# Optimization experiments

Measured on AMD Instinct MI355X. Metric: run time of the kernel, lower is better.

Reference implementation:

```python
import jax, jax.numpy as jnp
from jax import lax
import numpy as np

PROPAGATE = 3  # propagate_size; avg_pool2d(3,1,pad=1)*9 == 3x3 zero-padded sum pool
EPS = 1e-07


def setup_inputs() -> dict:
    key = jax.random.key(0)
    k1, k2 = jax.random.split(key)
    foreground = jax.random.normal(k1, (4, 64, 64, 64), dtype=jnp.float32)
    masks = jax.random.uniform(k2, (4, 1, 64, 64), dtype=jnp.float32)
    return {"foreground": foreground, "masks": masks}


def _sum_pool3x3(x):
    # x: [b, p, h, w]; 3x3 stride-1 zero-padded sum (== avg_pool2d(3,1,pad=1) * 9)
    return lax.reduce_window(x, 0.0, lax.add,
                             window_dimensions=(1, 1, PROPAGATE, PROPAGATE),
                             window_strides=(1, 1, 1, 1),
                             padding=[(0, 0), (0, 0), (1, 1), (1, 1)])


def reference(foreground, masks):
    # First-call forward of KnowledgeConsistentAttention (att_scores_prev is None;
    # masks/ratio are only stored as state and do not affect this output).
    bz, nc, h, w = foreground.shape
    # dynamic 1x1 kernels: one kernel per spatial location -> [b, h*w, nc]
    kern = foreground.reshape(bz, nc, h * w).transpose(0, 2, 1) + EPS
    kern = kern / jnp.sqrt(jnp.sum(kern ** 2, axis=-1, keepdims=True))
    # conv2d with per-image 1x1 kernels == per-pixel dot products
    scores = jnp.einsum('bpc,bcyx->bpyx', kern, foreground)  # [b, h*w, h, w]
    scores = _sum_pool3x3(scores)
    att = jax.nn.softmax(scores, axis=1)
    # conv_transpose2d with the same 1x1 kernels == weighted sum of kernels
    out = jnp.einsum('bpc,bpyx->bcyx', kern, att)  # [b, nc, h, w]
    return out
```

## Files before the change

kernel.cpp:

```cpp
#include <hip/hip_runtime.h>


typedef __bf16 bf16_t;
typedef __bf16 bf16x2 __attribute__((ext_vector_type(2)));
typedef __bf16 bf16x8 __attribute__((ext_vector_type(8)));
typedef float f32x4 __attribute__((ext_vector_type(4)));

#define HW_ 4096
#define CH 64

static __device__ __forceinline__ void gload_lds16(const void* gsrc, void* lds_dst) {
  __builtin_amdgcn_global_load_lds(
      (const __attribute__((address_space(1))) unsigned int*)gsrc,
      (__attribute__((address_space(3))) unsigned int*)lds_dst, 16, 0, 0);
}

static __device__ __forceinline__ int pack_bf16x2(float a, float b) {
  bf16x2 p; p[0] = (bf16_t)a; p[1] = (bf16_t)b;
  return __builtin_bit_cast(int, p);
}

__global__ __launch_bounds__(1024, 1) void kca_prep(const float* __restrict__ fg,
                                                    char* __restrict__ KpB,
                                                    char* __restrict__ KBB,
                                                    char* __restrict__ GtB) {
  const int b = blockIdx.x >> 6, y = blockIdx.x & 63;
  const int t = threadIdx.x;
  const float* F = fg + (size_t)b * (CH * HW_);

  __shared__ float  Ft[3 * 64 * 64];
  __shared__ bf16_t Ks[64 * 72];
  __shared__ bf16_t Gs[64 * 72];
  __shared__ float  red[16][64];
  __shared__ float  rn[64];

#pragma unroll
  for (int k = 0; k < 3; ++k) {
    const int o = t + k * 1024;
    const int r = o >> 10, c = (o >> 4) & 63, x4 = o & 15;
    const int gy = y - 1 + r;
    f32x4 v = {0.f, 0.f, 0.f, 0.f};
    if (gy >= 0 && gy <= 63) v = *(const f32x4*)(F + c * HW_ + gy * 64 + x4 * 4);
    *(f32x4*)&Ft[o * 4] = v;
  }
  __syncthreads();

  const int x = t & 63, c0 = t >> 6;
  float v4[4], g4[4], ssq = 0.f;
#pragma unroll
  for (int i = 0; i < 4; ++i) {
    const int c = c0 * 4 + i;
    const float v = Ft[4096 + c * 64 + x] + 1e-7f;
    v4[i] = v; ssq = fmaf(v, v, ssq);
    float s = 0.f;
#pragma unroll
    for (int r = 0; r < 3; ++r) {
      const float* row = &Ft[r * 4096 + c * 64];
      float vv = row[x];
      if (x > 0)  vv += row[x - 1];
      if (x < 63) vv += row[x + 1];
      s += vv;
    }
    g4[i] = s * 1.4426950408889634f;
  }
  red[c0][x] = ssq;
  __syncthreads();
  if (t < 512) red[t >> 6][t & 63] += red[(t >> 6) + 8][t & 63];
  __syncthreads();
  if (t < 256) red[t >> 6][t & 63] += red[(t >> 6) + 4][t & 63];
  __syncthreads();
  if (t < 64) rn[t] = 1.0f / sqrtf(red[0][t] + red[1][t] + red[2][t] + red[3][t]);
  __syncthreads();
  {
    const float rv = rn[x];
    bf16x2* ksp = (bf16x2*)((char*)Ks + x * 144 + c0 * 8);
    bf16x2* gsp = (bf16x2*)((char*)Gs + x * 144 + c0 * 8);
    bf16x2 k0; k0[0] = (bf16_t)(v4[0] * rv); k0[1] = (bf16_t)(v4[1] * rv);
    bf16x2 k1; k1[0] = (bf16_t)(v4[2] * rv); k1[1] = (bf16_t)(v4[3] * rv);
    bf16x2 g0; g0[0] = (bf16_t)g4[0]; g0[1] = (bf16_t)g4[1];
    bf16x2 g1; g1[0] = (bf16_t)g4[2]; g1[1] = (bf16_t)g4[3];
    ksp[0] = k0; ksp[1] = k1;
    gsp[0] = g0; gsp[1] = g1;
  }
  __syncthreads();

  char* Kp_b = KpB + (size_t)b * (HW_ * CH * 2) + (size_t)y * 8192;
  char* Gt_b = GtB + (size_t)b * (HW_ * CH * 2) + (size_t)y * 8192;
  char* KB_b = KBB + (size_t)b * (HW_ * CH * 2);
  if (t < 512) {
    const int row = t >> 3, colb = (t & 7) * 16;
    *(bf16x8*)(Kp_b + row * 128 + colb) = *(const bf16x8*)((char*)Ks + row * 144 + colb);
    const int tile = t >> 8;
    const int mt   = (t >> 6) & 3;
    const int ln   = t & 63;
    const int l15_ = ln & 15, lg_ = ln >> 4;
    bf16x8 kv;
#pragma unroll
    for (int j = 0; j < 8; ++j) {
      const int pl = tile * 32 + 16 * (j >> 2) + 4 * lg_ + (j & 3);
      kv[j] = Ks[pl * 72 + 16 * mt + l15_];
    }
    *(bf16x8*)(KB_b + (size_t)(2 * y + tile) * 4096 + mt * 1024 + ln * 16) = kv;
  } else {
    const int s = t - 512;
    const int row = s >> 3, colb = (s & 7) * 16;
    *(bf16x8*)(Gt_b + row * 128 + colb) = *(const bf16x8*)((char*)Gs + row * 144 + colb);
  }
}

__global__ __launch_bounds__(1024, 4) void kca_attn(const char* __restrict__ KpB,
                                                    const char* __restrict__ KBB,
                                                    const char* __restrict__ GtB,
                                                    float* __restrict__ out,
                                                    float* __restrict__ po1,
                                                    float* __restrict__ lw) {
  const int sw_id = ((blockIdx.x & 7) << 6) | (blockIdx.x >> 3);
  const int h = sw_id >> 8;
  const int b = (sw_id >> 6) & 3, y = sw_id & 63;
  const int t = threadIdx.x;
  const int lane = t & 63, w = t >> 6;
  const int g = w & 7;
  const int st = w >> 3;
  const int l15 = lane & 15, lg = lane >> 4;

  const char* Kp_b = KpB + (size_t)b * (HW_ * CH * 2);
  const char* KB_b = KBB + (size_t)b * (HW_ * CH * 2);
  const char* Gt_b = GtB + (size_t)b * (HW_ * CH * 2);
  float* dstO = (h ? po1 : out) + (size_t)b * (CH * HW_);

  __shared__ __align__(16) char SM[69632];
  __shared__ float mll[8][64];

  char* KpG = SM + g * 8192;

  bf16x8 qb00, qb01, qb10, qb11;
  {
    const char* qr0 = Gt_b + (size_t)(y * 64 + st * 32 + l15) * 128;
    const char* qr1 = qr0 + 16 * 128;
    qb00 = *(const bf16x8*)(qr0 + 16 * lg);
    qb01 = *(const bf16x8*)(qr0 + 64 + 16 * lg);
    qb10 = *(const bf16x8*)(qr1 + 16 * lg);
    qb11 = *(const bf16x8*)(qr1 + 64 + 16 * lg);
  }

  const int cA = st * 128 + lane, cB = cA + 64;
  const int rA1 = cA >> 3, rB1 = cB >> 3;
  const size_t kpoffA = (size_t)rA1 * 128 + (((cA & 7) * 16) ^ ((rA1 & 7) << 4));
  const size_t kpoffB = (size_t)rB1 * 128 + (((cB & 7) * 16) ^ ((rB1 & 7) << 4));

#define STAGE_KP(D, P0)                                                          \
  do {                                                                           \
    gload_lds16(Kp_b + (size_t)(P0) * 128 + kpoffA, KpG + (D) * 4096 + cA * 16); \
    gload_lds16(Kp_b + (size_t)(P0) * 128 + kpoffB, KpG + (D) * 4096 + cB * 16); \
  } while (0)

  f32x4 oaccT[2][4];
#pragma unroll
  for (int s = 0; s < 2; ++s)
#pragma unroll
    for (int mt = 0; mt < 4; ++mt) { oaccT[s][mt][0]=0.f; oaccT[s][mt][1]=0.f; oaccT[s][mt][2]=0.f; oaccT[s][mt][3]=0.f; }
  float lpart0 = 0.f, lpart1 = 0.f;

  const int pb0 = h * 2048 + g * 256;
  STAGE_KP(0, pb0);
  int cur = 0;
  for (int it = 0; it < 8; ++it) {
    __syncthreads();
    const char* kbp = KB_b + (size_t)((pb0 >> 5) + it) * 4096 + lane * 16;
    const bf16x8 kb0 = *(const bf16x8*)(kbp);
    const bf16x8 kb1 = *(const bf16x8*)(kbp + 1024);
    const bf16x8 kb2 = *(const bf16x8*)(kbp + 2048);
    const bf16x8 kb3 = *(const bf16x8*)(kbp + 3072);
    if (it + 1 < 8) STAGE_KP(cur ^ 1, pb0 + (it + 1) * 32);

    const char* kp = KpG + cur * 4096;
    f32x4 S[2][2];
#pragma unroll
    for (int f = 0; f < 2; ++f) {
      const int r = f * 16 + l15, swr = (r & 7) << 4;
      bf16x8 a0 = *(const bf16x8*)(kp + r * 128 + ((16 * lg) ^ swr));
      bf16x8 a1 = *(const bf16x8*)(kp + r * 128 + ((64 + 16 * lg) ^ swr));
      f32x4 z0 = {0.f, 0.f, 0.f, 0.f};
      z0 = __builtin_amdgcn_mfma_f32_16x16x32_bf16(a0, qb00, z0, 0, 0, 0);
      z0 = __builtin_amdgcn_mfma_f32_16x16x32_bf16(a1, qb01, z0, 0, 0, 0);
      S[0][f] = z0;
      f32x4 z1 = {0.f, 0.f, 0.f, 0.f};
      z1 = __builtin_amdgcn_mfma_f32_16x16x32_bf16(a0, qb10, z1, 0, 0, 0);
      z1 = __builtin_amdgcn_mfma_f32_16x16x32_bf16(a1, qb11, z1, 0, 0, 0);
      S[1][f] = z1;
    }

    union { int wd[4]; bf16x8 v; } pa0, pa1;
    {
      const float e0 = exp2f(S[0][0][0]), e1 = exp2f(S[0][0][1]);
      const float e2 = exp2f(S[0][0][2]), e3 = exp2f(S[0][0][3]);
      const float e4 = exp2f(S[0][1][0]), e5 = exp2f(S[0][1][1]);
      const float e6 = exp2f(S[0][1][2]), e7 = exp2f(S[0][1][3]);
      lpart0 += ((e0 + e1) + (e2 + e3)) + ((e4 + e5) + (e6 + e7));
      pa0.wd[0] = pack_bf16x2(e0, e1); pa0.wd[1] = pack_bf16x2(e2, e3);
      pa0.wd[2] = pack_bf16x2(e4, e5); pa0.wd[3] = pack_bf16x2(e6, e7);
    }
    {
      const float e0 = exp2f(S[1][0][0]), e1 = exp2f(S[1][0][1]);
      const float e2 = exp2f(S[1][0][2]), e3 = exp2f(S[1][0][3]);
      const float e4 = exp2f(S[1][1][0]), e5 = exp2f(S[1][1][1]);
      const float e6 = exp2f(S[1][1][2]), e7 = exp2f(S[1][1][3]);
      lpart1 += ((e0 + e1) + (e2 + e3)) + ((e4 + e5) + (e6 + e7));
      pa1.wd[0] = pack_bf16x2(e0, e1); pa1.wd[1] = pack_bf16x2(e2, e3);
      pa1.wd[2] = pack_bf16x2(e4, e5); pa1.wd[3] = pack_bf16x2(e6, e7);
    }

    oaccT[0][0] = __builtin_amdgcn_mfma_f32_16x16x32_bf16(pa0.v, kb0, oaccT[0][0], 0, 0, 0);
    oaccT[1][0] = __builtin_amdgcn_mfma_f32_16x16x32_bf16(pa1.v, kb0, oaccT[1][0], 0, 0, 0);
    oaccT[0][1] = __builtin_amdgcn_mfma_f32_16x16x32_bf16(pa0.v, kb1, oaccT[0][1], 0, 0, 0);
    oaccT[1][1] = __builtin_amdgcn_mfma_f32_16x16x32_bf16(pa1.v, kb1, oaccT[1][1], 0, 0, 0);
    oaccT[0][2] = __builtin_amdgcn_mfma_f32_16x16x32_bf16(pa0.v, kb2, oaccT[0][2], 0, 0, 0);
    oaccT[1][2] = __builtin_amdgcn_mfma_f32_16x16x32_bf16(pa1.v, kb2, oaccT[1][2], 0, 0, 0);
    oaccT[0][3] = __builtin_amdgcn_mfma_f32_16x16x32_bf16(pa0.v, kb3, oaccT[0][3], 0, 0, 0);
    oaccT[1][3] = __builtin_amdgcn_mfma_f32_16x16x32_bf16(pa1.v, kb3, oaccT[1][3], 0, 0, 0);
    cur ^= 1;
  }
#undef STAGE_KP

  lpart0 += __shfl_xor(lpart0, 16); lpart0 += __shfl_xor(lpart0, 32);
  lpart1 += __shfl_xor(lpart1, 16); lpart1 += __shfl_xor(lpart1, 32);
  if (lg == 0) {
    mll[g][st * 32 + l15]      = lpart0;
    mll[g][st * 32 + 16 + l15] = lpart1;
  }
  __syncthreads();
  if (t < 64) {
    float L = 0.f;
#pragma unroll
    for (int k = 0; k < 8; ++k) L += mll[k][t];
    lw[(size_t)((h * 4 + b) * 64 + y) * 64 + t] = L;
  }
  float* Rg = (float*)SM + (g >> 1) * 4352;
  if ((g & 1) == 0) {
#pragma unroll
    for (int s = 0; s < 2; ++s)
#pragma unroll
      for (int mt = 0; mt < 4; ++mt)
#pragma unroll
        for (int r = 0; r < 4; ++r)
          Rg[(16 * mt + l15) * 68 + st * 32 + s * 16 + 4 * lg + r] = oaccT[s][mt][r];
  }
  __syncthreads();
  if (g & 1) {
#pragma unroll
    for (int s = 0; s < 2; ++s)
#pragma unroll
      for (int mt = 0; mt < 4; ++mt)
#pragma unroll
        for (int r = 0; r < 4; ++r)
          Rg[(16 * mt + l15) * 68 + st * 32 + s * 16 + 4 * lg + r] += oaccT[s][mt][r];
  }
  __syncthreads();
  {
    const int c = t >> 4, q4 = (t & 15) * 4;
    const float* R0 = (const float*)SM;
    f32x4 v = *(const f32x4*)(R0 + c * 68 + q4);
    v += *(const f32x4*)(R0 + 4352 + c * 68 + q4);
    v += *(const f32x4*)(R0 + 8704 + c * 68 + q4);
    v += *(const f32x4*)(R0 + 13056 + c * 68 + q4);
    *(f32x4*)(dstO + (size_t)c * HW_ + y * 64 + q4) = v;
  }
}

__global__ __launch_bounds__(256, 8) void kca_reduce(float* __restrict__ out,
                                                     const float* __restrict__ po1,
                                                     const float* __restrict__ lw) {
  const size_t idx = ((size_t)blockIdx.x * 256 + threadIdx.x) * 4;
  const int b = (int)(idx >> 18);
  const int y = (int)((idx >> 6) & 63);
  const int q = (int)(idx & 63);
  const size_t lidx = (size_t)(b * 64 + y) * 64 + q;
  const f32x4 a  = *(const f32x4*)(out + idx);
  const f32x4 p  = *(const f32x4*)(po1 + idx);
  const f32x4 l0 = *(const f32x4*)(lw + lidx);
  const f32x4 l1 = *(const f32x4*)(lw + 16384 + lidx);
  f32x4 o;
#pragma unroll
  for (int j = 0; j < 4; ++j) o[j] = (a[j] + p[j]) * (1.0f / (l0[j] + l1[j]));
  *(f32x4*)(out + idx) = o;
}

extern "C" void kernel_launch(void* const* d_in, const int* in_sizes, int n_in,
                              void* d_out, int out_size, void* d_ws, size_t ws_size,
                              hipStream_t stream) {
  const float* fg = (const float*)d_in[0];
  float* out = (float*)d_out;
  char* ws = (char*)d_ws;
  char* Kp  = ws;
  char* KB  = ws + (2u << 20);
  char* Gt  = ws + (4u << 20);
  float* PO1 = (float*)(ws + (6u << 20));
  float* LW  = (float*)(ws + (10u << 20));
  hipLaunchKernelGGL(kca_prep, dim3(256), dim3(1024), 0, stream, fg, Kp, KB, Gt);
  hipLaunchKernelGGL(kca_attn, dim3(512), dim3(1024), 0, stream, Kp, KB, Gt, out, PO1, LW);
  hipLaunchKernelGGL(kca_reduce, dim3(1024), dim3(256), 0, stream, out, PO1, LW);
}
```

Before: 54.36 us.

## Split attention key range four ways with 256-thread blocks and direct global loads

Restructures the attention kernel from 512 blocks of 1024 threads (two key halves, LDS-staged K tiles via async global-to-LDS loads) to 1024 blocks of 256 threads. Each block covers a quarter of the keys, and each wave handles all 64 query pixels of a row, reading K fragments straight from global/L2. Cross-wave partial sums are combined in a smaller LDS buffer. The reduce kernel now sums four partial outputs and four partial denominators. This drops the per-iteration block barriers and LDS staging and raises block count for better CU spread. In exchange it adds more global/L2 traffic, uses a larger partial-output workspace, and makes the final reduction heavier.

```diff
diff --git a/kernel.cpp b/kernel.cpp
--- a/kernel.cpp
+++ b/kernel.cpp
@@ -8,12 +8,6 @@
 
 #define HW_ 4096
 #define CH 64
-
-static __device__ __forceinline__ void gload_lds16(const void* gsrc, void* lds_dst) {
-  __builtin_amdgcn_global_load_lds(
-      (const __attribute__((address_space(1))) unsigned int*)gsrc,
-      (__attribute__((address_space(3))) unsigned int*)lds_dst, 16, 0, 0);
-}
 
 static __device__ __forceinline__ int pack_bf16x2(float a, float b) {
   bf16x2 p; p[0] = (bf16_t)a; p[1] = (bf16_t)b;
@@ -108,180 +102,147 @@
   }
 }
 
-__global__ __launch_bounds__(1024, 4) void kca_attn(const char* __restrict__ KpB,
-                                                    const char* __restrict__ KBB,
-                                                    const char* __restrict__ GtB,
-                                                    float* __restrict__ out,
-                                                    float* __restrict__ po1,
-                                                    float* __restrict__ lw) {
-  const int sw_id = ((blockIdx.x & 7) << 6) | (blockIdx.x >> 3);
-  const int h = sw_id >> 8;
-  const int b = (sw_id >> 6) & 3, y = sw_id & 63;
+__global__ __launch_bounds__(256, 1) void kca_attn(const char* __restrict__ KpB,
+                                                   const char* __restrict__ KBB,
+                                                   const char* __restrict__ GtB,
+                                                   float* __restrict__ out,
+                                                   float* __restrict__ po,
+                                                   float* __restrict__ lw) {
+  const int sw = ((blockIdx.x & 7) << 7) | (blockIdx.x >> 3);
+  const int h = sw >> 8;
+  const int b = (sw >> 6) & 3, y = sw & 63;
   const int t = threadIdx.x;
   const int lane = t & 63, w = t >> 6;
-  const int g = w & 7;
-  const int st = w >> 3;
   const int l15 = lane & 15, lg = lane >> 4;
 
   const char* Kp_b = KpB + (size_t)b * (HW_ * CH * 2);
   const char* KB_b = KBB + (size_t)b * (HW_ * CH * 2);
   const char* Gt_b = GtB + (size_t)b * (HW_ * CH * 2);
-  float* dstO = (h ? po1 : out) + (size_t)b * (CH * HW_);
-
-  __shared__ __align__(16) char SM[69632];
-  __shared__ float mll[8][64];
-
-  char* KpG = SM + g * 8192;
-
-  bf16x8 qb00, qb01, qb10, qb11;
-  {
-    const char* qr0 = Gt_b + (size_t)(y * 64 + st * 32 + l15) * 128;
-    const char* qr1 = qr0 + 16 * 128;
-    qb00 = *(const bf16x8*)(qr0 + 16 * lg);
-    qb01 = *(const bf16x8*)(qr0 + 64 + 16 * lg);
-    qb10 = *(const bf16x8*)(qr1 + 16 * lg);
-    qb11 = *(const bf16x8*)(qr1 + 64 + 16 * lg);
-  }
-
-  const int cA = st * 128 + lane, cB = cA + 64;
-  const int rA1 = cA >> 3, rB1 = cB >> 3;
-  const size_t kpoffA = (size_t)rA1 * 128 + (((cA & 7) * 16) ^ ((rA1 & 7) << 4));
-  const size_t kpoffB = (size_t)rB1 * 128 + (((cB & 7) * 16) ^ ((rB1 & 7) << 4));
-
-#define STAGE_KP(D, P0)                                                          \
-  do {                                                                           \
-    gload_lds16(Kp_b + (size_t)(P0) * 128 + kpoffA, KpG + (D) * 4096 + cA * 16); \
-    gload_lds16(Kp_b + (size_t)(P0) * 128 + kpoffB, KpG + (D) * 4096 + cB * 16); \
-  } while (0)
-
-  f32x4 oaccT[2][4];
-#pragma unroll
-  for (int s = 0; s < 2; ++s)
-#pragma unroll
-    for (int mt = 0; mt < 4; ++mt) { oaccT[s][mt][0]=0.f; oaccT[s][mt][1]=0.f; oaccT[s][mt][2]=0.f; oaccT[s][mt][3]=0.f; }
-  float lpart0 = 0.f, lpart1 = 0.f;
-
-  const int pb0 = h * 2048 + g * 256;
-  STAGE_KP(0, pb0);
-  int cur = 0;
+
+  __shared__ float Rcomb[2][64 * 72];
+  __shared__ float mll[4][64];
+
+  bf16x8 qb[4][2];
+#pragma unroll
+  for (int qs = 0; qs < 4; ++qs) {
+    const char* qr = Gt_b + (size_t)(y * 64 + qs * 16 + l15) * 128 + 16 * lg;
+    qb[qs][0] = *(const bf16x8*)qr;
+    qb[qs][1] = *(const bf16x8*)(qr + 64);
+  }
+
+  f32x4 oaccT[4][4];
+#pragma unroll
+  for (int qs = 0; qs < 4; ++qs)
+#pragma unroll
+    for (int mt = 0; mt < 4; ++mt) { oaccT[qs][mt][0]=0.f; oaccT[qs][mt][1]=0.f; oaccT[qs][mt][2]=0.f; oaccT[qs][mt][3]=0.f; }
+  float lpart[4] = {0.f, 0.f, 0.f, 0.f};
+
+  const int pbase = h * 1024 + w * 256;
   for (int it = 0; it < 8; ++it) {
-    __syncthreads();
-    const char* kbp = KB_b + (size_t)((pb0 >> 5) + it) * 4096 + lane * 16;
+    const int p0 = pbase + it * 32;
+    const char* kbp = KB_b + (size_t)(p0 >> 5) * 4096 + lane * 16;
     const bf16x8 kb0 = *(const bf16x8*)(kbp);
     const bf16x8 kb1 = *(const bf16x8*)(kbp + 1024);
     const bf16x8 kb2 = *(const bf16x8*)(kbp + 2048);
     const bf16x8 kb3 = *(const bf16x8*)(kbp + 3072);
-    if (it + 1 < 8) STAGE_KP(cur ^ 1, pb0 + (it + 1) * 32);
-
-    const char* kp = KpG + cur * 4096;
-    f32x4 S[2][2];
+
+    union PU { int wd[4]; bf16x8 v; } pa[4];
+
 #pragma unroll
     for (int f = 0; f < 2; ++f) {
-      const int r = f * 16 + l15, swr = (r & 7) << 4;
-      bf16x8 a0 = *(const bf16x8*)(kp + r * 128 + ((16 * lg) ^ swr));
-      bf16x8 a1 = *(const bf16x8*)(kp + r * 128 + ((64 + 16 * lg) ^ swr));
-      f32x4 z0 = {0.f, 0.f, 0.f, 0.f};
-      z0 = __builtin_amdgcn_mfma_f32_16x16x32_bf16(a0, qb00, z0, 0, 0, 0);
-      z0 = __builtin_amdgcn_mfma_f32_16x16x32_bf16(a1, qb01, z0, 0, 0, 0);
-      S[0][f] = z0;
-      f32x4 z1 = {0.f, 0.f, 0.f, 0.f};
-      z1 = __builtin_amdgcn_mfma_f32_16x16x32_bf16(a0, qb10, z1, 0, 0, 0);
-      z1 = __builtin_amdgcn_mfma_f32_16x16x32_bf16(a1, qb11, z1, 0, 0, 0);
-      S[1][f] = z1;
-    }
-
-    union { int wd[4]; bf16x8 v; } pa0, pa1;
-    {
-      const float e0 = exp2f(S[0][0][0]), e1 = exp2f(S[0][0][1]);
-      const float e2 = exp2f(S[0][0][2]), e3 = exp2f(S[0][0][3]);
-      const float e4 = exp2f(S[0][1][0]), e5 = exp2f(S[0][1][1]);
-      const float e6 = exp2f(S[0][1][2]), e7 = exp2f(S[0][1][3]);
-      lpart0 += ((e0 + e1) + (e2 + e3)) + ((e4 + e5) + (e6 + e7));
-      pa0.wd[0] = pack_bf16x2(e0, e1); pa0.wd[1] = pack_bf16x2(e2, e3);
-      pa0.wd[2] = pack_bf16x2(e4, e5); pa0.wd[3] = pack_bf16x2(e6, e7);
-    }
-    {
-      const float e0 = exp2f(S[1][0][0]), e1 = exp2f(S[1][0][1]);
-      const float e2 = exp2f(S[1][0][2]), e3 = exp2f(S[1][0][3]);
-      const float e4 = exp2f(S[1][1][0]), e5 = exp2f(S[1][1][1]);
-      const float e6 = exp2f(S[1][1][2]), e7 = exp2f(S[1][1][3]);
-      lpart1 += ((e0 + e1) + (e2 + e3)) + ((e4 + e5) + (e6 + e7));
-      pa1.wd[0] = pack_bf16x2(e0, e1); pa1.wd[1] = pack_bf16x2(e2, e3);
-      pa1.wd[2] = pack_bf16x2(e4, e5); pa1.wd[3] = pack_bf16x2(e6, e7);
-    }
-
-    oaccT[0][0] = __builtin_amdgcn_mfma_f32_16x16x32_bf16(pa0.v, kb0, oaccT[0][0], 0, 0, 0);
-    oaccT[1][0] = __builtin_amdgcn_mfma_f32_16x16x32_bf16(pa1.v, kb0, oaccT[1][0], 0, 0, 0);
-    oaccT[0][1] = __builtin_amdgcn_mfma_f32_16x16x32_bf16(pa0.v, kb1, oaccT[0][1], 0, 0, 0);
-    oaccT[1][1] = __builtin_amdgcn_mfma_f32_16x16x32_bf16(pa1.v, kb1, oaccT[1][1], 0, 0, 0);
-    oaccT[0][2] = __builtin_amdgcn_mfma_f32_16x16x32_bf16(pa0.v, kb2, oaccT[0][2], 0, 0, 0);
-    oaccT[1][2] = __builtin_amdgcn_mfma_f32_16x16x32_bf16(pa1.v, kb2, oaccT[1][2], 0, 0, 0);
-    oaccT[0][3] = __builtin_amdgcn_mfma_f32_16x16x32_bf16(pa0.v, kb3, oaccT[0][3], 0, 0, 0);
-    oaccT[1][3] = __builtin_amdgcn_mfma_f32_16x16x32_bf16(pa1.v, kb3, oaccT[1][3], 0, 0, 0);
-    cur ^= 1;
-  }
-#undef STAGE_KP
-
-  lpart0 += __shfl_xor(lpart0, 16); lpart0 += __shfl_xor(lpart0, 32);
-  lpart1 += __shfl_xor(lpart1, 16); lpart1 += __shfl_xor(lpart1, 32);
+      const char* ar = Kp_b + (size_t)(p0 + f * 16 + l15) * 128 + 16 * lg;
+      const bf16x8 a0 = *(const bf16x8*)(ar);
+      const bf16x8 a1 = *(const bf16x8*)(ar + 64);
+#pragma unroll
+      for (int qs = 0; qs < 4; ++qs) {
+        f32x4 z = {0.f, 0.f, 0.f, 0.f};
+        z = __builtin_amdgcn_mfma_f32_16x16x32_bf16(a0, qb[qs][0], z, 0, 0, 0);
+        z = __builtin_amdgcn_mfma_f32_16x16x32_bf16(a1, qb[qs][1], z, 0, 0, 0);
+        const float e0 = exp2f(z[0]), e1 = exp2f(z[1]);
+        const float e2 = exp2f(z[2]), e3 = exp2f(z[3]);
+        lpart[qs] += (e0 + e1) + (e2 + e3);
+        pa[qs].wd[2 * f + 0] = pack_bf16x2(e0, e1);
+        pa[qs].wd[2 * f + 1] = pack_bf16x2(e2, e3);
+      }
+    }
+
+#pragma unroll
+    for (int qs = 0; qs < 4; ++qs) {
+      oaccT[qs][0] = __builtin_amdgcn_mfma_f32_16x16x32_bf16(pa[qs].v, kb0, oaccT[qs][0], 0, 0, 0);
+      oaccT[qs][1] = __builtin_amdgcn_mfma_f32_16x16x32_bf16(pa[qs].v, kb1, oaccT[qs][1], 0, 0, 0);
+      oaccT[qs][2] = __builtin_amdgcn_mfma_f32_16x16x32_bf16(pa[qs].v, kb2, oaccT[qs][2], 0, 0, 0);
+      oaccT[qs][3] = __builtin_amdgcn_mfma_f32_16x16x32_bf16(pa[qs].v, kb3, oaccT[qs][3], 0, 0, 0);
+    }
+  }
+
+#pragma unroll
+  for (int qs = 0; qs < 4; ++qs) {
+    lpart[qs] += __shfl_xor(lpart[qs], 16);
+    lpart[qs] += __shfl_xor(lpart[qs], 32);
+  }
   if (lg == 0) {
-    mll[g][st * 32 + l15]      = lpart0;
-    mll[g][st * 32 + 16 + l15] = lpart1;
+#pragma unroll
+    for (int qs = 0; qs < 4; ++qs) mll[w][qs * 16 + l15] = lpart[qs];
+  }
+  float* Rg = &Rcomb[w & 1][0];
+  if (w < 2) {
+#pragma unroll
+    for (int qs = 0; qs < 4; ++qs)
+#pragma unroll
+      for (int mt = 0; mt < 4; ++mt)
+#pragma unroll
+        for (int r = 0; r < 4; ++r)
+          Rg[(16 * mt + l15) * 72 + qs * 16 + 4 * lg + r] = oaccT[qs][mt][r];
+  }
+  __syncthreads();
+  if (w >= 2) {
+#pragma unroll
+    for (int qs = 0; qs < 4; ++qs)
+#pragma unroll
+      for (int mt = 0; mt < 4; ++mt)
+#pragma unroll
+        for (int r = 0; r < 4; ++r)
+          Rg[(16 * mt + l15) * 72 + qs * 16 + 4 * lg + r] += oaccT[qs][mt][r];
   }
   __syncthreads();
   if (t < 64) {
-    float L = 0.f;
-#pragma unroll
-    for (int k = 0; k < 8; ++k) L += mll[k][t];
-    lw[(size_t)((h * 4 + b) * 64 + y) * 64 + t] = L;
-  }
-  float* Rg = (float*)SM + (g >> 1) * 4352;
-  if ((g & 1) == 0) {
-#pragma unroll
-    for (int s = 0; s < 2; ++s)
-#pragma unroll
-      for (int mt = 0; mt < 4; ++mt)
-#pragma unroll
-        for (int r = 0; r < 4; ++r)
-          Rg[(16 * mt + l15) * 68 + st * 32 + s * 16 + 4 * lg + r] = oaccT[s][mt][r];
-  }
-  __syncthreads();
-  if (g & 1) {
-#pragma unroll
-    for (int s = 0; s < 2; ++s)
-#pragma unroll
-      for (int mt = 0; mt < 4; ++mt)
-#pragma unroll
-        for (int r = 0; r < 4; ++r)
-          Rg[(16 * mt + l15) * 68 + st * 32 + s * 16 + 4 * lg + r] += oaccT[s][mt][r];
-  }
-  __syncthreads();
+    const float L = mll[0][t] + mll[1][t] + mll[2][t] + mll[3][t];
+    lw[(size_t)h * 16384 + (size_t)(b * 64 + y) * 64 + t] = L;
+  }
   {
-    const int c = t >> 4, q4 = (t & 15) * 4;
-    const float* R0 = (const float*)SM;
-    f32x4 v = *(const f32x4*)(R0 + c * 68 + q4);
-    v += *(const f32x4*)(R0 + 4352 + c * 68 + q4);
-    v += *(const f32x4*)(R0 + 8704 + c * 68 + q4);
-    v += *(const f32x4*)(R0 + 13056 + c * 68 + q4);
-    *(f32x4*)(dstO + (size_t)c * HW_ + y * 64 + q4) = v;
+    const int c = t >> 2, q16 = (t & 3) * 16;
+    float* dst = (h ? po + (size_t)(h - 1) * 4 * CH * HW_ : out)
+               + (size_t)b * CH * HW_ + (size_t)c * HW_ + y * 64 + q16;
+    const float* r0 = &Rcomb[0][c * 72 + q16];
+    const float* r1 = &Rcomb[1][c * 72 + q16];
+#pragma unroll
+    for (int j = 0; j < 4; ++j) {
+      f32x4 v = *(const f32x4*)(r0 + 4 * j);
+      v += *(const f32x4*)(r1 + 4 * j);
+      *(f32x4*)(dst + 4 * j) = v;
+    }
   }
 }
 
 __global__ __launch_bounds__(256, 8) void kca_reduce(float* __restrict__ out,
-                                                     const float* __restrict__ po1,
+                                                     const float* __restrict__ po,
                                                      const float* __restrict__ lw) {
   const size_t idx = ((size_t)blockIdx.x * 256 + threadIdx.x) * 4;
   const int b = (int)(idx >> 18);
   const int y = (int)((idx >> 6) & 63);
   const int q = (int)(idx & 63);
   const size_t lidx = (size_t)(b * 64 + y) * 64 + q;
-  const f32x4 a  = *(const f32x4*)(out + idx);
-  const f32x4 p  = *(const f32x4*)(po1 + idx);
-  const f32x4 l0 = *(const f32x4*)(lw + lidx);
-  const f32x4 l1 = *(const f32x4*)(lw + 16384 + lidx);
+  f32x4 v = *(const f32x4*)(out + idx);
+  v += *(const f32x4*)(po + idx);
+  v += *(const f32x4*)(po + 1048576 + idx);
+  v += *(const f32x4*)(po + 2097152 + idx);
+  f32x4 l = *(const f32x4*)(lw + lidx);
+  l += *(const f32x4*)(lw + 16384 + lidx);
+  l += *(const f32x4*)(lw + 32768 + lidx);
+  l += *(const f32x4*)(lw + 49152 + lidx);
   f32x4 o;
 #pragma unroll
-  for (int j = 0; j < 4; ++j) o[j] = (a[j] + p[j]) * (1.0f / (l0[j] + l1[j]));
+  for (int j = 0; j < 4; ++j) o[j] = v[j] * (1.0f / l[j]);
   *(f32x4*)(out + idx) = o;
 }
 
@@ -294,9 +255,9 @@
   char* Kp  = ws;
   char* KB  = ws + (2u << 20);
   char* Gt  = ws + (4u << 20);
-  float* PO1 = (float*)(ws + (6u << 20));
-  float* LW  = (float*)(ws + (10u << 20));
+  float* PO = (float*)(ws + (6u << 20));
+  float* LW = (float*)(ws + (18u << 20));
   hipLaunchKernelGGL(kca_prep, dim3(256), dim3(1024), 0, stream, fg, Kp, KB, Gt);
-  hipLaunchKernelGGL(kca_attn, dim3(512), dim3(1024), 0, stream, Kp, KB, Gt, out, PO1, LW);
-  hipLaunchKernelGGL(kca_reduce, dim3(1024), dim3(256), 0, stream, out, PO1, LW);
-}
+  hipLaunchKernelGGL(kca_attn, dim3(1024), dim3(256), 0, stream, Kp, KB, Gt, out, PO, LW);
+  hipLaunchKernelGGL(kca_reduce, dim3(1024), dim3(256), 0, stream, out, PO, LW);
+}
```

After: 57.17 us. +5.2%, slower.
